# Performance work log

Hardware: AMD Instinct MI355X
Metric: run time of the kernel (lower is better)

## Reference

```python
import jax, jax.numpy as jnp
import numpy as np

WH, WW = 7, 7
N_TOK = WH * WW


def _buffers():
    # relative_coords_table: [1, 2*WH-1, 2*WW-1, 2], Swin-V2 log-spaced coords
    ch = np.arange(-(WH - 1), WH, dtype=np.float32)
    cw = np.arange(-(WW - 1), WW, dtype=np.float32)
    t = np.stack(np.meshgrid(ch, cw, indexing='ij'), axis=-1)[None]
    t[..., 0] /= (WH - 1)
    t[..., 1] /= (WW - 1)
    t *= 8.0
    t = np.sign(t) * np.log2(np.abs(t) + 1.0) / np.log2(8.0)
    # relative_position_index: [N, N]
    coords = np.stack(np.meshgrid(np.arange(WH), np.arange(WW), indexing='ij'))
    cf = coords.reshape(2, -1)
    rc = (cf[:, :, None] - cf[:, None, :]).transpose(1, 2, 0).astype(np.int32)
    rc[..., 0] += WH - 1
    rc[..., 1] += WW - 1
    rc[..., 0] *= 2 * WW - 1
    idx = rc.sum(-1)
    return jnp.asarray(t, jnp.float32), jnp.asarray(idx, jnp.int32)


def setup_inputs() -> dict:
    key = jax.random.key(0)
    ks = jax.random.split(key, 10)
    C, H = 384, 12
    B_, nW = 2048, 64
    rel_table, rel_index = _buffers()
    s = 0.02
    return {
        'x': jax.random.normal(ks[0], (B_, N_TOK, C), jnp.float32),
        'mask': jax.random.normal(ks[1], (nW, N_TOK, N_TOK), jnp.float32),
        'qkv_w': jax.random.normal(ks[2], (3 * C, C), jnp.float32) * s,
        'q_bias': jnp.zeros((C,), jnp.float32),
        'v_bias': jnp.zeros((C,), jnp.float32),
        'logit_scale': jnp.full((H, 1, 1), np.log(10.0), jnp.float32),
        'cpb_w1': jax.random.normal(ks[3], (512, 2), jnp.float32) * s,
        'cpb_b1': jnp.zeros((512,), jnp.float32),
        'cpb_w2': jax.random.normal(ks[4], (H, 512), jnp.float32) * s,
        'proj_w': jax.random.normal(ks[5], (C, C), jnp.float32) * s,
        'proj_b': jnp.zeros((C,), jnp.float32),
        'rel_table': rel_table,
        'rel_index': rel_index,
    }


def reference(x, mask, qkv_w, q_bias, v_bias, logit_scale, cpb_w1, cpb_b1,
              cpb_w2, proj_w, proj_b, rel_table, rel_index):
    B_, N, C = x.shape
    H = logit_scale.shape[0]
    Dh = C // H
    nW = mask.shape[0]
    # qkv projection with q/v bias, zero bias for k
    qkv_bias = jnp.concatenate([q_bias, jnp.zeros_like(v_bias), v_bias])
    qkv = x @ qkv_w.T + qkv_bias                       # [B, N, 3C]
    qkv = qkv.reshape(B_, N, 3, H, Dh).transpose(2, 0, 3, 1, 4)
    q, k, v = qkv[0], qkv[1], qkv[2]                    # [B, H, N, Dh]
    # per-head clamped logit scale
    ls = jnp.exp(jnp.minimum(logit_scale, np.log(1.0 / 0.01)))  # [H,1,1]
    # continuous relative position bias via small MLP
    tbl = jax.nn.relu(rel_table @ cpb_w1.T + cpb_b1) @ cpb_w2.T  # [1,13,13,H]
    tbl = tbl.reshape(-1, H)
    rpb = tbl[rel_index.reshape(-1)].reshape(N, N, H).transpose(2, 0, 1)
    rpb = 16.0 * jax.nn.sigmoid(rpb)                    # [H, N, N]
    # cosine attention (kernel uses norm + 1e-6 in denominator)
    qn = q / (jnp.sqrt(jnp.sum(q * q, -1, keepdims=True)) + 1e-6)
    kn = k / (jnp.sqrt(jnp.sum(k * k, -1, keepdims=True)) + 1e-6)
    attn = jnp.einsum('bhnd,bhmd->bhnm', qn, kn) * ls[None]
    attn = attn + rpb[None]
    # shift mask: window index w = batch_index % nW
    attn = attn.reshape(B_ // nW, nW, H, N, N) + mask[None, :, None]
    attn = attn.reshape(B_, H, N, N)
    # stable softmax with kernel's +1e-6 in denominator
    m = jnp.max(attn, -1, keepdims=True)
    e = jnp.exp(attn - m)
    p = e / (jnp.sum(e, -1, keepdims=True) + 1e-6)
    out = jnp.einsum('bhnm,bhmd->bhnd', p, v)           # [B, H, N, Dh]
    out = out.transpose(0, 2, 1, 3).reshape(B_, N, C)
    return out @ proj_w.T + proj_b
```

## Files before the change

### kernel.cpp

```cpp
#include <hip/hip_runtime.h>
#include <hip/hip_bf16.h>

typedef __attribute__((ext_vector_type(8))) short bf16x8;
typedef __attribute__((ext_vector_type(4))) float f32x4;
typedef __attribute__((ext_vector_type(16))) float f32x16;
typedef __attribute__((ext_vector_type(8))) unsigned short u16x8;
typedef unsigned short ushort_t;

#define DEVFN static __device__ __forceinline__

DEVFN ushort_t f2bf(float f) {
  unsigned int u = __builtin_bit_cast(unsigned int, f);
  u += 0x7FFFu + ((u >> 16) & 1u);
  return (ushort_t)(u >> 16);
}

DEVFN unsigned int cvtpk_bf16(float lo, float hi) {
  unsigned int r;
  asm("v_cvt_pk_bf16_f32 %0, %1, %2" : "=v"(r) : "v"(lo), "v"(hi));
  return r;
}

DEVFN void gload_lds16(const ushort_t* g, ushort_t* l) {
  __builtin_amdgcn_global_load_lds(
      (const __attribute__((address_space(1))) void*)g,
      (__attribute__((address_space(3))) void*)l, 16, 0, 0);
}

DEVFN int xcd_swz(int bid, int nwg) {
  int q = nwg >> 3, r = nwg & 7;
  int xcd = bid & 7, u = bid >> 3;
  return (xcd < r ? xcd * (q + 1) : r * (q + 1) + (xcd - r) * q) + u;
}

__global__ void k_prep_w(const float* __restrict__ qkv_w, const float* __restrict__ proj_w,
                         const float* __restrict__ q_bias, const float* __restrict__ v_bias,
                         ushort_t* __restrict__ qkv_wb, ushort_t* __restrict__ proj_wb,
                         float* __restrict__ qkv_bias) {
  int gid = blockIdx.x * blockDim.x + threadIdx.x;
  int stride = gridDim.x * blockDim.x;
  for (int i = gid; i < 1152 * 384; i += stride) qkv_wb[i] = f2bf(qkv_w[i]);
  for (int i = gid; i < 384 * 384; i += stride) proj_wb[i] = f2bf(proj_w[i]);
  for (int i = gid; i < 1152; i += stride)
    qkv_bias[i] = (i < 384) ? q_bias[i] : ((i < 768) ? 0.f : v_bias[i - 768]);
}

__global__ void k_xb(const float* __restrict__ x, ushort_t* __restrict__ xb, long n4) {
  long gid = (long)blockIdx.x * blockDim.x + threadIdx.x;
  long stride = (long)gridDim.x * blockDim.x;
  for (long i = gid; i < n4; i += stride) {
    float4 v = reinterpret_cast<const float4*>(x)[i];
    unsigned long long pk = (unsigned long long)f2bf(v.x) |
                            ((unsigned long long)f2bf(v.y) << 16) |
                            ((unsigned long long)f2bf(v.z) << 32) |
                            ((unsigned long long)f2bf(v.w) << 48);
    reinterpret_cast<unsigned long long*>(xb)[i] = pk;
  }
}

__global__ void k_prep_cpb(const float* __restrict__ rel_table, const float* __restrict__ cpb_w1,
                           const float* __restrict__ cpb_b1, const float* __restrict__ cpb_w2,
                           const float* __restrict__ logit_scale,
                           float* __restrict__ tbl, float* __restrict__ ls) {
  int lane = threadIdx.x;
  if (blockIdx.x == 169) {
    if (lane < 12) ls[lane] = __expf(fminf(logit_scale[lane], 4.605170185988092f));
    return;
  }
  int row = blockIdx.x;
  float t0 = rel_table[row * 2 + 0], t1 = rel_table[row * 2 + 1];
  float acc[12];
#pragma unroll
  for (int h = 0; h < 12; h++) acc[h] = 0.f;
  for (int j = lane; j < 512; j += 64) {
    float hj = fmaxf(cpb_w1[j * 2] * t0 + cpb_w1[j * 2 + 1] * t1 + cpb_b1[j], 0.f);
#pragma unroll
    for (int h = 0; h < 12; h++) acc[h] += cpb_w2[h * 512 + j] * hj;
  }
#pragma unroll
  for (int h = 0; h < 12; h++) {
    float v = acc[h];
    v += __shfl_xor(v, 1);  v += __shfl_xor(v, 2);  v += __shfl_xor(v, 4);
    v += __shfl_xor(v, 8);  v += __shfl_xor(v, 16); v += __shfl_xor(v, 32);
    if (lane == 0) tbl[row * 12 + h] = v;
  }
}

__global__ void k_prep_comb(const float* __restrict__ tbl, const int* __restrict__ rel_index,
                            const float* __restrict__ mask, float* __restrict__ comb) {
  int gid = blockIdx.x * blockDim.x + threadIdx.x;
  if (gid >= 64 * 12 * 2401) return;
  int ij = gid % 2401;
  int h = (gid / 2401) % 12;
  int w = gid / (2401 * 12);
  float t = tbl[rel_index[ij] * 12 + h];
  comb[gid] = 16.f / (1.f + __expf(-t)) + mask[w * 2401 + ij];
}

__global__ void __launch_bounds__(256, 4) k_qkv(const ushort_t* __restrict__ xb,
                                                const ushort_t* __restrict__ wb,
                                                const float* __restrict__ bias,
                                                const float* __restrict__ lsb,
                                                ushort_t* __restrict__ qkvn, int nmb) {
  __shared__ __align__(16) ushort_t As[128][64];
  __shared__ __align__(16) ushort_t Bs[128][64];
  const int tid = threadIdx.x;
  const int lane = tid & 63, wid = tid >> 6;
  const int wm = wid >> 1, wn = wid & 1;
  const int l15 = lane & 15, g = lane >> 4;
  const int t = xcd_swz(blockIdx.x, nmb * 9);
  const int m0 = (t / 9) * 128, n0 = (t % 9) * 128;
  f32x4 acc[4][4] = {};

  const int rb_ = (wid << 3) + (lane >> 3);
  const int cg_ = (lane & 7) ^ (rb_ & 7);
  const size_t so_ = (size_t)rb_ * 384 + cg_ * 8;
  const int lo_ = wid * 512;

#define QKV_STAGE(kk)                                                        \
  {                                                                          \
    const ushort_t* ga = xb + (size_t)m0 * 384 + (kk) * 64;                  \
    const ushort_t* gb = wb + (size_t)n0 * 384 + (kk) * 64;                  \
    _Pragma("unroll")                                                        \
    for (int it = 0; it < 4; it++) {                                         \
      gload_lds16(ga + so_ + (size_t)it * 12288, &As[0][0] + lo_ + it * 2048);\
      gload_lds16(gb + so_ + (size_t)it * 12288, &Bs[0][0] + lo_ + it * 2048);\
    }                                                                        \
  }

  for (int kk = 0; kk < 6; kk++) {
    __syncthreads();
    QKV_STAGE(kk);
    __syncthreads();
#pragma unroll
    for (int ks = 0; ks < 64; ks += 32) {
      const int cxor = (ks >> 3) + g;
      bf16x8 a[4], b[4];
#pragma unroll
      for (int mi = 0; mi < 4; mi++) {
        int row = wm * 64 + mi * 16 + l15;
        a[mi] = *reinterpret_cast<const bf16x8*>(&As[row][(cxor ^ (row & 7)) * 8]);
      }
#pragma unroll
      for (int ni = 0; ni < 4; ni++) {
        int row = wn * 64 + ni * 16 + l15;
        b[ni] = *reinterpret_cast<const bf16x8*>(&Bs[row][(cxor ^ (row & 7)) * 8]);
      }
#pragma unroll
      for (int mi = 0; mi < 4; mi++)
#pragma unroll
        for (int ni = 0; ni < 4; ni++)
          acc[mi][ni] = __builtin_amdgcn_mfma_f32_16x16x32_bf16(a[mi], b[ni], acc[mi][ni], 0, 0, 0);
    }
  }
#undef QKV_STAGE
  const int colbase = n0 + wn * 64;
  const int which = colbase / 384;
  const float scl0 = (which == 0) ? lsb[(colbase >> 5)] : 1.f;
  const float scl1 = (which == 0) ? lsb[(colbase >> 5) + 1] : 1.f;
  float bs[4];
#pragma unroll
  for (int ni = 0; ni < 4; ni++) bs[ni] = bias[colbase + ni * 16 + l15];
#pragma unroll
  for (int mi = 0; mi < 4; mi++) {
#pragma unroll
    for (int r = 0; r < 4; r++) {
      float v[4];
#pragma unroll
      for (int ni = 0; ni < 4; ni++) v[ni] = acc[mi][ni][r] + bs[ni];
      if (which < 2) {
        float ss0 = v[0] * v[0] + v[1] * v[1];
        float ss1 = v[2] * v[2] + v[3] * v[3];
        ss0 += __shfl_xor(ss0, 1); ss1 += __shfl_xor(ss1, 1);
        ss0 += __shfl_xor(ss0, 2); ss1 += __shfl_xor(ss1, 2);
        ss0 += __shfl_xor(ss0, 4); ss1 += __shfl_xor(ss1, 4);
        ss0 += __shfl_xor(ss0, 8); ss1 += __shfl_xor(ss1, 8);
        float rn0 = scl0 / (sqrtf(ss0) + 1e-6f);
        float rn1 = scl1 / (sqrtf(ss1) + 1e-6f);
        v[0] *= rn0; v[1] *= rn0; v[2] *= rn1; v[3] *= rn1;
      }
      int row = m0 + wm * 64 + mi * 16 + g * 4 + r;
      size_t base = (size_t)row * 1152 + colbase + l15;
#pragma unroll
      for (int ni = 0; ni < 4; ni++) qkvn[base + ni * 16] = f2bf(v[ni]);
    }
  }
}

__global__ void __launch_bounds__(256, 4) k_attn(const ushort_t* __restrict__ qkvn,
                                                 const float* __restrict__ comb,
                                                 ushort_t* __restrict__ attn,
                                                 int win_base, int nk) {
  __shared__ float comb_s[2401];
  __shared__ __align__(16) ushort_t Vt[4][32][72];
  const int tid = threadIdx.x;
  const int lane = tid & 63, wv = tid >> 6;
  const int l31 = lane & 31, hi = lane >> 5;
  const int h = blockIdx.y;
  const int wloc = blockIdx.x & 63;
  const int k = (blockIdx.x >> 6) * 4 + wv;
  const bool active = k < nk;
  const int w_abs = (win_base + wloc) & 63;

  {
    const float* ct = comb + ((size_t)w_abs * 12 + h) * 2401;
    for (int i = tid; i < 2401; i += 256) comb_s[i] = ct[i];
  }

  const size_t rowbase = (size_t)(wloc + 64 * k) * 49;

  if (active) {
#pragma unroll
    for (int pass = 0; pass < 4; pass++) {
      int t = pass * 16 + (lane >> 2);
      int d0 = (lane & 3) * 8;
      u16x8 v = {};
      if (t < 49)
        v = *reinterpret_cast<const u16x8*>(&qkvn[(rowbase + t) * 1152 + 768 + h * 32 + d0]);
#pragma unroll
      for (int j = 0; j < 8; j++) Vt[wv][d0 + j][t] = v[j];
    }
  }
  __syncthreads();
  if (!active) return;

  bf16x8 qf[2][2], kf[2][2];
#pragma unroll
  for (int b = 0; b < 2; b++) {
    int t = b * 32 + l31; if (t > 48) t = 48;
    size_t rb = (rowbase + t) * 1152 + h * 32 + hi * 8;
#pragma unroll
    for (int ks = 0; ks < 2; ks++) {
      qf[b][ks] = *reinterpret_cast<const bf16x8*>(&qkvn[rb + ks * 16]);
      kf[b][ks] = *reinterpret_cast<const bf16x8*>(&qkvn[rb + 384 + ks * 16]);
    }
  }
  f32x16 S[2][2] = {};
#pragma unroll
  for (int a = 0; a < 2; a++)
#pragma unroll
    for (int b = 0; b < 2; b++) {
      S[a][b] = __builtin_amdgcn_mfma_f32_32x32x16_bf16(kf[a][0], qf[b][0], S[a][b], 0, 0, 0);
      S[a][b] = __builtin_amdgcn_mfma_f32_32x32x16_bf16(kf[a][1], qf[b][1], S[a][b], 0, 0, 0);
    }

#pragma unroll
  for (int b = 0; b < 2; b++) {
    const int qt = b * 32 + l31;
    const int qi = qt > 48 ? 48 : qt;
    const float* crow_p = &comb_s[qi * 49];
    float m = -3.0e38f;
#pragma unroll
    for (int a = 0; a < 2; a++)
#pragma unroll
      for (int r = 0; r < 16; r++) {
        int kt = a * 32 + (r & 3) + 8 * (r >> 2) + 4 * hi;
        float v = (kt < 49) ? (S[a][b][r] + crow_p[kt]) : -3.0e38f;
        S[a][b][r] = v;
        m = fmaxf(m, v);
      }
    m = fmaxf(m, __shfl_xor(m, 32));
    float s = 0.f;
#pragma unroll
    for (int a = 0; a < 2; a++)
#pragma unroll
      for (int r = 0; r < 16; r++) {
        float e = __expf(S[a][b][r] - m);
        S[a][b][r] = e;
        s += e;
      }
    s += __shfl_xor(s, 32);
    const float inv = 1.f / (s + 1e-6f);
    unsigned int pkk[2][4][2];
#pragma unroll
    for (int a = 0; a < 2; a++)
#pragma unroll
      for (int c = 0; c < 4; c++) {
        pkk[a][c][0] = cvtpk_bf16(S[a][b][c * 4 + 0] * inv, S[a][b][c * 4 + 1] * inv);
        pkk[a][c][1] = cvtpk_bf16(S[a][b][c * 4 + 2] * inv, S[a][b][c * 4 + 3] * inv);
      }
    f32x16 O = {};
#pragma unroll
    for (int a = 0; a < 2; a++)
#pragma unroll
      for (int ks = 0; ks < 2; ks++) {
        unsigned int s0 = hi ? pkk[a][2 * ks][0] : pkk[a][2 * ks + 1][0];
        unsigned int s1 = hi ? pkk[a][2 * ks][1] : pkk[a][2 * ks + 1][1];
        unsigned int r0 = __shfl_xor(s0, 32);
        unsigned int r1 = __shfl_xor(s1, 32);
        unsigned int w0 = hi ? r0 : pkk[a][2 * ks][0];
        unsigned int w1 = hi ? r1 : pkk[a][2 * ks][1];
        unsigned int w2 = hi ? pkk[a][2 * ks + 1][0] : r0;
        unsigned int w3 = hi ? pkk[a][2 * ks + 1][1] : r1;
        uint4 wq = {w0, w1, w2, w3};
        bf16x8 pa = __builtin_bit_cast(bf16x8, wq);
        bf16x8 vb = *reinterpret_cast<const bf16x8*>(&Vt[wv][l31][a * 32 + ks * 16 + hi * 8]);
        O = __builtin_amdgcn_mfma_f32_32x32x16_bf16(pa, vb, O, 0, 0, 0);
      }
#pragma unroll
    for (int r = 0; r < 16; r++) {
      int qrow = b * 32 + (r & 3) + 8 * (r >> 2) + 4 * hi;
      if (qrow < 49)
        attn[(rowbase + qrow) * 384 + h * 32 + l31] = f2bf(O[r]);
    }
  }
}

__global__ void __launch_bounds__(256, 4) k_proj(const ushort_t* __restrict__ a,
                                                 const ushort_t* __restrict__ wb,
                                                 const float* __restrict__ pbias,
                                                 float* __restrict__ out, int nmb) {
  __shared__ __align__(16) ushort_t As[128][64];
  __shared__ __align__(16) ushort_t Bs[128][64];
  const int tid = threadIdx.x;
  const int lane = tid & 63, wid = tid >> 6;
  const int wm = wid >> 1, wn = wid & 1;
  const int l15 = lane & 15, g = lane >> 4;
  const int t = xcd_swz(blockIdx.x, nmb * 3);
  const int m0 = (t / 3) * 128, n0 = (t % 3) * 128;
  f32x4 acc[4][4] = {};

  const int rb_ = (wid << 3) + (lane >> 3);
  const int cg_ = (lane & 7) ^ (rb_ & 7);
  const size_t so_ = (size_t)rb_ * 384 + cg_ * 8;
  const int lo_ = wid * 512;

#define PRJ_STAGE(kk)                                                        \
  {                                                                          \
    const ushort_t* ga = a + (size_t)m0 * 384 + (kk) * 64;                   \
    const ushort_t* gb = wb + (size_t)n0 * 384 + (kk) * 64;                  \
    _Pragma("unroll")                                                        \
    for (int it = 0; it < 4; it++) {                                         \
      gload_lds16(ga + so_ + (size_t)it * 12288, &As[0][0] + lo_ + it * 2048);\
      gload_lds16(gb + so_ + (size_t)it * 12288, &Bs[0][0] + lo_ + it * 2048);\
    }                                                                        \
  }

  for (int kk = 0; kk < 6; kk++) {
    __syncthreads();
    PRJ_STAGE(kk);
    __syncthreads();
#pragma unroll
    for (int ks = 0; ks < 64; ks += 32) {
      const int cxor = (ks >> 3) + g;
      bf16x8 av[4], bv[4];
#pragma unroll
      for (int mi = 0; mi < 4; mi++) {
        int row = wm * 64 + mi * 16 + l15;
        av[mi] = *reinterpret_cast<const bf16x8*>(&As[row][(cxor ^ (row & 7)) * 8]);
      }
#pragma unroll
      for (int ni = 0; ni < 4; ni++) {
        int row = wn * 64 + ni * 16 + l15;
        bv[ni] = *reinterpret_cast<const bf16x8*>(&Bs[row][(cxor ^ (row & 7)) * 8]);
      }
#pragma unroll
      for (int mi = 0; mi < 4; mi++)
#pragma unroll
        for (int ni = 0; ni < 4; ni++)
          acc[mi][ni] = __builtin_amdgcn_mfma_f32_16x16x32_bf16(av[mi], bv[ni], acc[mi][ni], 0, 0, 0);
    }
  }
#undef PRJ_STAGE
  const int colbase = n0 + wn * 64;
  float bs[4];
#pragma unroll
  for (int ni = 0; ni < 4; ni++) bs[ni] = pbias[colbase + ni * 16 + l15];
#pragma unroll
  for (int mi = 0; mi < 4; mi++)
#pragma unroll
    for (int r = 0; r < 4; r++) {
      int row = m0 + wm * 64 + mi * 16 + g * 4 + r;
#pragma unroll
      for (int ni = 0; ni < 4; ni++)
        out[(size_t)row * 384 + colbase + ni * 16 + l15] = acc[mi][ni][r] + bs[ni];
    }
}

extern "C" void kernel_launch(void* const* d_in, const int* in_sizes, int n_in,
                              void* d_out, int out_size, void* d_ws, size_t ws_size,
                              hipStream_t stream) {
  const float* x        = (const float*)d_in[0];
  const float* mask     = (const float*)d_in[1];
  const float* qkv_w    = (const float*)d_in[2];
  const float* q_bias   = (const float*)d_in[3];
  const float* v_bias   = (const float*)d_in[4];
  const float* logit_sc = (const float*)d_in[5];
  const float* cpb_w1   = (const float*)d_in[6];
  const float* cpb_b1   = (const float*)d_in[7];
  const float* cpb_w2   = (const float*)d_in[8];
  const float* proj_w   = (const float*)d_in[9];
  const float* proj_b   = (const float*)d_in[10];
  const float* rel_tab  = (const float*)d_in[11];
  const int*   rel_idx  = (const int*)d_in[12];
  float* out = (float*)d_out;

  char* p = (char*)d_ws;
  auto carve = [&](size_t bytes) { char* r = p; p += (bytes + 255) & ~(size_t)255; return r; };
  ushort_t* qkv_wb  = (ushort_t*)carve(1152 * 384 * 2);
  ushort_t* proj_wb = (ushort_t*)carve(384 * 384 * 2);
  float* qkv_bias   = (float*)carve(1152 * 4);
  float* tbl        = (float*)carve(169 * 12 * 4);
  float* lsb        = (float*)carve(12 * 4);
  float* comb       = (float*)carve((size_t)64 * 12 * 2401 * 4);
  size_t fixed = (size_t)(p - (char*)d_ws);
  size_t avail = ws_size > fixed ? ws_size - fixed : 0;

  int nc = 1;
  while (nc < 16) {
    size_t per = ((size_t)(2048 / nc)) * 49 * (384 + 1152 + 384) * 2 + (1 << 20);
    if (per <= avail) break;
    nc *= 2;
  }
  const int nwin = 2048 / nc;
  const size_t Mc = (size_t)nwin * 49;
  ushort_t* xbuf  = (ushort_t*)carve(Mc * 384 * 2);
  ushort_t* qkvn  = (ushort_t*)carve(Mc * 1152 * 2);
  ushort_t* attnb = (ushort_t*)carve(Mc * 384 * 2);
  const int nmb = (int)(Mc / 128);
  const int nk = nwin >> 6;

  k_prep_w<<<dim3(512), dim3(256), 0, stream>>>(qkv_w, proj_w, q_bias, v_bias, qkv_wb, proj_wb, qkv_bias);
  k_prep_cpb<<<dim3(170), dim3(64), 0, stream>>>(rel_tab, cpb_w1, cpb_b1, cpb_w2, logit_sc, tbl, lsb);
  k_prep_comb<<<dim3((64 * 12 * 2401 + 255) / 256), dim3(256), 0, stream>>>(tbl, rel_idx, mask, comb);

  for (int c = 0; c < nc; c++) {
    size_t roff = (size_t)c * Mc;
    k_xb<<<dim3(2048), dim3(256), 0, stream>>>(x + roff * 384, xbuf, (long)(Mc * 384 / 4));
    k_qkv<<<dim3(nmb * 9), dim3(256), 0, stream>>>(xbuf, qkv_wb, qkv_bias, lsb, qkvn, nmb);
    k_attn<<<dim3(64 * ((nk + 3) / 4), 12), dim3(256), 0, stream>>>(qkvn, comb, attnb, c * nwin, nk);
    k_proj<<<dim3(nmb * 3), dim3(256), 0, stream>>>(attnb, proj_wb, proj_b, out + roff * 384, nmb);
  }
}
```

Before: 401.7 us.

## Double-buffer LDS tiles in QKV and projection GEMMs with explicit waitcnt pipelining

Both GEMM kernels now use two LDS buffers per operand and a fully unrolled prologue/steady-state schedule, so the global-to-LDS load for the next K slice is issued while MFMAs run on the current one. Explicit vmcnt/lgkmcnt waits and raw barriers replace the paired __syncthreads. The aim is to hide global load latency behind compute. LDS per block doubles, so the launch bounds drop from 4 to 2 blocks per CU, which may reduce occupancy-based latency hiding.

After: 439.0 us. +9.3%, slower.

```diff
diff --git a/kernel.cpp b/kernel.cpp
--- a/kernel.cpp
+++ b/kernel.cpp
@@ -26,6 +26,12 @@
       (const __attribute__((address_space(1))) void*)g,
       (__attribute__((address_space(3))) void*)l, 16, 0, 0);
 }
+
+#define WAIT_VM(n) do { asm volatile("s_waitcnt vmcnt(" #n ")" ::: "memory"); \
+                        __builtin_amdgcn_sched_barrier(0); } while (0)
+#define WAIT_LGKM0 do { asm volatile("s_waitcnt lgkmcnt(0)" ::: "memory"); \
+                        __builtin_amdgcn_sched_barrier(0); } while (0)
+#define RAW_BAR __builtin_amdgcn_s_barrier()
 
 DEVFN int xcd_swz(int bid, int nwg) {
   int q = nwg >> 3, r = nwg & 7;
@@ -97,13 +103,13 @@
   comb[gid] = 16.f / (1.f + __expf(-t)) + mask[w * 2401 + ij];
 }
 
-__global__ void __launch_bounds__(256, 4) k_qkv(const ushort_t* __restrict__ xb,
+__global__ void __launch_bounds__(256, 2) k_qkv(const ushort_t* __restrict__ xb,
                                                 const ushort_t* __restrict__ wb,
                                                 const float* __restrict__ bias,
                                                 const float* __restrict__ lsb,
                                                 ushort_t* __restrict__ qkvn, int nmb) {
-  __shared__ __align__(16) ushort_t As[128][64];
-  __shared__ __align__(16) ushort_t Bs[128][64];
+  __shared__ __align__(16) ushort_t As[2][128][64];
+  __shared__ __align__(16) ushort_t Bs[2][128][64];
   const int tid = threadIdx.x;
   const int lane = tid & 63, wid = tid >> 6;
   const int wm = wid >> 1, wn = wid & 1;
@@ -116,44 +122,64 @@
   const int cg_ = (lane & 7) ^ (rb_ & 7);
   const size_t so_ = (size_t)rb_ * 384 + cg_ * 8;
   const int lo_ = wid * 512;
-
-#define QKV_STAGE(kk)                                                        \
+  const ushort_t* gA = xb + (size_t)m0 * 384 + so_;
+  const ushort_t* gB = wb + (size_t)n0 * 384 + so_;
+
+#define QKV_STAGE(buf, kk)                                                   \
   {                                                                          \
-    const ushort_t* ga = xb + (size_t)m0 * 384 + (kk) * 64;                  \
-    const ushort_t* gb = wb + (size_t)n0 * 384 + (kk) * 64;                  \
     _Pragma("unroll")                                                        \
     for (int it = 0; it < 4; it++) {                                         \
-      gload_lds16(ga + so_ + (size_t)it * 12288, &As[0][0] + lo_ + it * 2048);\
-      gload_lds16(gb + so_ + (size_t)it * 12288, &Bs[0][0] + lo_ + it * 2048);\
+      gload_lds16(gA + (kk) * 64 + (size_t)it * 12288,                       \
+                  &As[buf][0][0] + lo_ + it * 2048);                         \
+      gload_lds16(gB + (kk) * 64 + (size_t)it * 12288,                       \
+                  &Bs[buf][0][0] + lo_ + it * 2048);                         \
     }                                                                        \
   }
 
-  for (int kk = 0; kk < 6; kk++) {
-    __syncthreads();
-    QKV_STAGE(kk);
-    __syncthreads();
-#pragma unroll
-    for (int ks = 0; ks < 64; ks += 32) {
-      const int cxor = (ks >> 3) + g;
-      bf16x8 a[4], b[4];
-#pragma unroll
-      for (int mi = 0; mi < 4; mi++) {
-        int row = wm * 64 + mi * 16 + l15;
-        a[mi] = *reinterpret_cast<const bf16x8*>(&As[row][(cxor ^ (row & 7)) * 8]);
-      }
-#pragma unroll
-      for (int ni = 0; ni < 4; ni++) {
-        int row = wn * 64 + ni * 16 + l15;
-        b[ni] = *reinterpret_cast<const bf16x8*>(&Bs[row][(cxor ^ (row & 7)) * 8]);
-      }
-#pragma unroll
-      for (int mi = 0; mi < 4; mi++)
-#pragma unroll
-        for (int ni = 0; ni < 4; ni++)
-          acc[mi][ni] = __builtin_amdgcn_mfma_f32_16x16x32_bf16(a[mi], b[ni], acc[mi][ni], 0, 0, 0);
-    }
-  }
+#define QKV_COMPUTE(buf)                                                     \
+  {                                                                          \
+    _Pragma("unroll")                                                        \
+    for (int ks = 0; ks < 64; ks += 32) {                                    \
+      const int cxor = (ks >> 3) + g;                                        \
+      bf16x8 a[4], b[4];                                                     \
+      _Pragma("unroll")                                                      \
+      for (int mi = 0; mi < 4; mi++) {                                       \
+        int row = wm * 64 + mi * 16 + l15;                                   \
+        a[mi] = *reinterpret_cast<const bf16x8*>(                            \
+            &As[buf][row][(cxor ^ (row & 7)) * 8]);                          \
+      }                                                                      \
+      _Pragma("unroll")                                                      \
+      for (int ni = 0; ni < 4; ni++) {                                       \
+        int row = wn * 64 + ni * 16 + l15;                                   \
+        b[ni] = *reinterpret_cast<const bf16x8*>(                            \
+            &Bs[buf][row][(cxor ^ (row & 7)) * 8]);                          \
+      }                                                                      \
+      _Pragma("unroll")                                                      \
+      for (int mi = 0; mi < 4; mi++)                                         \
+        _Pragma("unroll")                                                    \
+        for (int ni = 0; ni < 4; ni++)                                       \
+          acc[mi][ni] = __builtin_amdgcn_mfma_f32_16x16x32_bf16(             \
+              a[mi], b[ni], acc[mi][ni], 0, 0, 0);                           \
+    }                                                                        \
+  }
+
+  QKV_STAGE(0, 0);
+  QKV_STAGE(1, 1);
+  WAIT_VM(8); RAW_BAR;
+  QKV_COMPUTE(0); WAIT_LGKM0; RAW_BAR;
+  QKV_STAGE(0, 2); WAIT_VM(8); RAW_BAR;
+  QKV_COMPUTE(1); WAIT_LGKM0; RAW_BAR;
+  QKV_STAGE(1, 3); WAIT_VM(8); RAW_BAR;
+  QKV_COMPUTE(0); WAIT_LGKM0; RAW_BAR;
+  QKV_STAGE(0, 4); WAIT_VM(8); RAW_BAR;
+  QKV_COMPUTE(1); WAIT_LGKM0; RAW_BAR;
+  QKV_STAGE(1, 5); WAIT_VM(8); RAW_BAR;
+  QKV_COMPUTE(0); WAIT_LGKM0; RAW_BAR;
+  WAIT_VM(0); RAW_BAR;
+  QKV_COMPUTE(1);
 #undef QKV_STAGE
+#undef QKV_COMPUTE
+
   const int colbase = n0 + wn * 64;
   const int which = colbase / 384;
   const float scl0 = (which == 0) ? lsb[(colbase >> 5)] : 1.f;
@@ -306,12 +332,12 @@
   }
 }
 
-__global__ void __launch_bounds__(256, 4) k_proj(const ushort_t* __restrict__ a,
+__global__ void __launch_bounds__(256, 2) k_proj(const ushort_t* __restrict__ a,
                                                  const ushort_t* __restrict__ wb,
                                                  const float* __restrict__ pbias,
                                                  float* __restrict__ out, int nmb) {
-  __shared__ __align__(16) ushort_t As[128][64];
-  __shared__ __align__(16) ushort_t Bs[128][64];
+  __shared__ __align__(16) ushort_t As[2][128][64];
+  __shared__ __align__(16) ushort_t Bs[2][128][64];
   const int tid = threadIdx.x;
   const int lane = tid & 63, wid = tid >> 6;
   const int wm = wid >> 1, wn = wid & 1;
@@ -324,44 +350,64 @@
   const int cg_ = (lane & 7) ^ (rb_ & 7);
   const size_t so_ = (size_t)rb_ * 384 + cg_ * 8;
   const int lo_ = wid * 512;
-
-#define PRJ_STAGE(kk)                                                        \
+  const ushort_t* gA = a + (size_t)m0 * 384 + so_;
+  const ushort_t* gB = wb + (size_t)n0 * 384 + so_;
+
+#define PRJ_STAGE(buf, kk)                                                   \
   {                                                                          \
-    const ushort_t* ga = a + (size_t)m0 * 384 + (kk) * 64;                   \
-    const ushort_t* gb = wb + (size_t)n0 * 384 + (kk) * 64;                  \
     _Pragma("unroll")                                                        \
     for (int it = 0; it < 4; it++) {                                         \
-      gload_lds16(ga + so_ + (size_t)it * 12288, &As[0][0] + lo_ + it * 2048);\
-      gload_lds16(gb + so_ + (size_t)it * 12288, &Bs[0][0] + lo_ + it * 2048);\
+      gload_lds16(gA + (kk) * 64 + (size_t)it * 12288,                       \
+                  &As[buf][0][0] + lo_ + it * 2048);                         \
+      gload_lds16(gB + (kk) * 64 + (size_t)it * 12288,                       \
+                  &Bs[buf][0][0] + lo_ + it * 2048);                         \
     }                                                                        \
   }
 
-  for (int kk = 0; kk < 6; kk++) {
-    __syncthreads();
-    PRJ_STAGE(kk);
-    __syncthreads();
-#pragma unroll
-    for (int ks = 0; ks < 64; ks += 32) {
-      const int cxor = (ks >> 3) + g;
-      bf16x8 av[4], bv[4];
-#pragma unroll
-      for (int mi = 0; mi < 4; mi++) {
-        int row = wm * 64 + mi * 16 + l15;
-        av[mi] = *reinterpret_cast<const bf16x8*>(&As[row][(cxor ^ (row & 7)) * 8]);
-      }
-#pragma unroll
-      for (int ni = 0; ni < 4; ni++) {
-        int row = wn * 64 + ni * 16 + l15;
-        bv[ni] = *reinterpret_cast<const bf16x8*>(&Bs[row][(cxor ^ (row & 7)) * 8]);
-      }
-#pragma unroll
-      for (int mi = 0; mi < 4; mi++)
-#pragma unroll
-        for (int ni = 0; ni < 4; ni++)
-          acc[mi][ni] = __builtin_amdgcn_mfma_f32_16x16x32_bf16(av[mi], bv[ni], acc[mi][ni], 0, 0, 0);
-    }
-  }
+#define PRJ_COMPUTE(buf)                                                     \
+  {                                                                          \
+    _Pragma("unroll")                                                        \
+    for (int ks = 0; ks < 64; ks += 32) {                                    \
+      const int cxor = (ks >> 3) + g;                                        \
+      bf16x8 av[4], bv[4];                                                   \
+      _Pragma("unroll")                                                      \
+      for (int mi = 0; mi < 4; mi++) {                                       \
+        int row = wm * 64 + mi * 16 + l15;                                   \
+        av[mi] = *reinterpret_cast<const bf16x8*>(                           \
+            &As[buf][row][(cxor ^ (row & 7)) * 8]);                          \
+      }                                                                      \
+      _Pragma("unroll")                                                      \
+      for (int ni = 0; ni < 4; ni++) {                                       \
+        int row = wn * 64 + ni * 16 + l15;                                   \
+        bv[ni] = *reinterpret_cast<const bf16x8*>(                           \
+            &Bs[buf][row][(cxor ^ (row & 7)) * 8]);                          \
+      }                                                                      \
+      _Pragma("unroll")                                                      \
+      for (int mi = 0; mi < 4; mi++)                                         \
+        _Pragma("unroll")                                                    \
+        for (int ni = 0; ni < 4; ni++)                                       \
+          acc[mi][ni] = __builtin_amdgcn_mfma_f32_16x16x32_bf16(             \
+              av[mi], bv[ni], acc[mi][ni], 0, 0, 0);                         \
+    }                                                                        \
+  }
+
+  PRJ_STAGE(0, 0);
+  PRJ_STAGE(1, 1);
+  WAIT_VM(8); RAW_BAR;
+  PRJ_COMPUTE(0); WAIT_LGKM0; RAW_BAR;
+  PRJ_STAGE(0, 2); WAIT_VM(8); RAW_BAR;
+  PRJ_COMPUTE(1); WAIT_LGKM0; RAW_BAR;
+  PRJ_STAGE(1, 3); WAIT_VM(8); RAW_BAR;
+  PRJ_COMPUTE(0); WAIT_LGKM0; RAW_BAR;
+  PRJ_STAGE(0, 4); WAIT_VM(8); RAW_BAR;
+  PRJ_COMPUTE(1); WAIT_LGKM0; RAW_BAR;
+  PRJ_STAGE(1, 5); WAIT_VM(8); RAW_BAR;
+  PRJ_COMPUTE(0); WAIT_LGKM0; RAW_BAR;
+  WAIT_VM(0); RAW_BAR;
+  PRJ_COMPUTE(1);
 #undef PRJ_STAGE
+#undef PRJ_COMPUTE
+
   const int colbase = n0 + wn * 64;
   float bs[4];
 #pragma unroll
```
